# Performance work log

Measured on AMD Instinct MI355X. Metric: run time of the kernel, lower is better.

Reference implementation:

```python
import jax, jax.numpy as jnp
import numpy as np

BN_EPS = 1e-5


def setup_inputs() -> dict:
    key = jax.random.key(0)
    ks = jax.random.split(key, 8)
    B, C, H, W = 8, 256, 64, 64
    Cqk = C // 8  # query/key channels = out_channels // 8
    x = jax.random.normal(ks[0], (B, C, H, W), dtype=jnp.float32)
    # 1x1 convs == per-pixel matmuls; kaiming-normal-ish scale
    wq = jax.random.normal(ks[1], (Cqk, C), dtype=jnp.float32) * np.sqrt(2.0 / C)
    bq = jnp.zeros((Cqk,), dtype=jnp.float32)
    wk = jax.random.normal(ks[2], (Cqk, C), dtype=jnp.float32) * np.sqrt(2.0 / C)
    bk = jnp.zeros((Cqk,), dtype=jnp.float32)
    wv = jax.random.normal(ks[3], (C, C), dtype=jnp.float32) * np.sqrt(2.0 / C)
    bv = jnp.zeros((C,), dtype=jnp.float32)
    # gamma is initialized to 0 in the original; use a small nonzero value so
    # the attention path actually contributes (and has nontrivial gradients)
    gamma = jnp.full((1,), 0.5, dtype=jnp.float32)
    bn_weight = jnp.ones((C,), dtype=jnp.float32)
    bn_bias = jnp.zeros((C,), dtype=jnp.float32)
    return {"x": x, "wq": wq, "bq": bq, "wk": wk, "bk": bk,
            "wv": wv, "bv": bv, "gamma": gamma,
            "bn_weight": bn_weight, "bn_bias": bn_bias}


def reference(x, wq, bq, wk, bk, wv, bv, gamma, bn_weight, bn_bias):
    B, C, H, W = x.shape
    N = H * W
    xf = x.reshape(B, C, N)  # (B, C, N)
    # 1x1 conv projections as channel matmuls
    q = jnp.einsum('oc,bcn->bno', wq, xf) + bq            # (B, N, Cqk)
    k = jnp.einsum('oc,bcn->bon', wk, xf) + bk[:, None]   # (B, Cqk, N)
    v = jnp.einsum('oc,bcn->bon', wv, xf) + bv[:, None]   # (B, C, N)
    # attention[b, i, j] = softmax_j(q_i . k_j)  -- full N x N matrix
    scores = jnp.einsum('bno,bom->bnm', q, k)             # (B, N, N)
    attn = jax.nn.softmax(scores, axis=2)
    # out[b, c, i] = sum_j v[b, c, j] * attn[b, i, j]
    out = jnp.einsum('bcj,bij->bci', v, attn)             # (B, C, N)
    out = out.reshape(B, C, H, W)
    out = gamma[0] * out + x
    # BatchNorm2d in training mode: batch statistics over (B, H, W)
    mean = jnp.mean(out, axis=(0, 2, 3), keepdims=True)
    var = jnp.var(out, axis=(0, 2, 3), keepdims=True)
    out = (out - mean) * jax.lax.rsqrt(var + BN_EPS)
    out = out * bn_weight[None, :, None, None] + bn_bias[None, :, None, None]
    return jax.nn.relu(out)
```

## Files before the change

kernel.cpp:

```cpp
#include <hip/hip_runtime.h>
#include <stdint.h>

#define B_ 8
#define C_ 256
#define N_ 4096
#define CQK 32

typedef __attribute__((ext_vector_type(8))) _Float16 f16x8;
typedef __attribute__((ext_vector_type(4))) float f32x4;

__device__ __forceinline__ unsigned short f2bf_rne(float f) {
  unsigned u = __builtin_bit_cast(unsigned, f);
  u += 0x7FFFu + ((u >> 16) & 1u);
  return (unsigned short)(u >> 16);
}

__global__ __launch_bounds__(256) void xpose_kernel(
    const float* __restrict__ x, _Float16* __restrict__ xT)
{
  __shared__ float xs[64 * 129];
  const int t  = threadIdx.x;
  const int blk = blockIdx.x;
  const int nt = blk & 31;
  const int ct = (blk >> 5) & 3;
  const int b  = blk >> 7;
  const int c0 = ct * 64, n0 = nt * 128;

  #pragma unroll
  for (int p = 0; p < 8; ++p) {
    int cc = p * 8 + (t >> 5);
    int nn = (t & 31) * 4;
    float4 v = *(const float4*)(x + ((size_t)(b * C_ + c0 + cc)) * N_ + n0 + nn);
    xs[cc * 129 + nn]     = v.x;
    xs[cc * 129 + nn + 1] = v.y;
    xs[cc * 129 + nn + 2] = v.z;
    xs[cc * 129 + nn + 3] = v.w;
  }
  __syncthreads();
  #pragma unroll
  for (int p = 0; p < 4; ++p) {
    int id = p * 256 + t;
    int cchunk = id & 7, n = id >> 3;
    _Float16 h[8];
    #pragma unroll
    for (int j = 0; j < 8; ++j) h[j] = (_Float16)xs[(cchunk * 8 + j) * 129 + n];
    *(f16x8*)(xT + ((size_t)(b * N_) + n0 + n) * C_ + c0 + cchunk * 8) = *(f16x8*)h;
  }
}

__global__ __launch_bounds__(256) void wconv_kernel(
    const float* __restrict__ wq, const float* __restrict__ wk,
    const float* __restrict__ wv, _Float16* __restrict__ wf)
{
  int idx = blockIdx.x * 256 + threadIdx.x;
  int e = idx * 4;
  int o = e >> 8, c = e & 255;
  const float* src;
  if (o < 32)      src = wq + o * 256 + c;
  else if (o < 64) src = wk + (o - 32) * 256 + c;
  else             src = wv + (o - 64) * 256 + c;
  float4 v = *(const float4*)src;
  _Float16 h[4] = {(_Float16)v.x, (_Float16)v.y, (_Float16)v.z, (_Float16)v.w};
  *(uint2*)(wf + e) = *(uint2*)h;
}

__global__ __launch_bounds__(256, 4) void proj_gemm_kernel(
    const _Float16* __restrict__ xT, const _Float16* __restrict__ wf,
    const float* __restrict__ bq, const float* __restrict__ bk,
    const float* __restrict__ bv,
    _Float16* __restrict__ qf, _Float16* __restrict__ kf,
    _Float16* __restrict__ vout)
{
  const int t = threadIdx.x, lane = t & 63;
  const int w = t >> 6;
  const int l15 = lane & 15, q4 = lane >> 4;
  const int blk = blockIdx.x;
  const int otile = blk % 5;
  const int nt = blk / 5;
  const int b  = nt >> 5;
  const int n0 = (nt & 31) * 128;
  const int o0w = (w & 1) * 32;
  const int n0w = (w >> 1) * 64;

  f32x4 acc[2][4];
  const f32x4 zf = {0.f, 0.f, 0.f, 0.f};
  #pragma unroll
  for (int a = 0; a < 2; ++a)
    #pragma unroll
    for (int bb = 0; bb < 4; ++bb) acc[a][bb] = zf;

  const _Float16* wbase = wf + (size_t)(otile * 64 + o0w) * 256;
  const _Float16* xbase = xT + ((size_t)(b * N_) + n0 + n0w) * C_;

  #pragma unroll
  for (int kc = 0; kc < 8; ++kc) {
    f16x8 af[2], bfr[4];
    #pragma unroll
    for (int ob = 0; ob < 2; ++ob)
      af[ob] = *(const f16x8*)(wbase + (ob * 16 + l15) * 256 + kc * 32 + q4 * 8);
    #pragma unroll
    for (int nb = 0; nb < 4; ++nb)
      bfr[nb] = *(const f16x8*)(xbase + (nb * 16 + l15) * 256 + kc * 32 + q4 * 8);
    #pragma unroll
    for (int ob = 0; ob < 2; ++ob)
      #pragma unroll
      for (int nb = 0; nb < 4; ++nb)
        acc[ob][nb] = __builtin_amdgcn_mfma_f32_16x16x32_f16(af[ob], bfr[nb], acc[ob][nb], 0, 0, 0);
  }

  if (otile == 0) {
    _Float16* dst = (o0w == 0) ? qf : kf;
    const float* bias = (o0w == 0) ? bq : bk;
    const float qsc = (o0w == 0) ? 1.4426950408889634f : 1.0f;
    #pragma unroll
    for (int ob = 0; ob < 2; ++ob) {
      float4 b4 = *(const float4*)(bias + ob * 16 + q4 * 4);
      #pragma unroll
      for (int nb = 0; nb < 4; ++nb) {
        int pixel = n0 + n0w + nb * 16 + l15;
        _Float16 h[4];
        h[0] = (_Float16)((acc[ob][nb][0] + b4.x) * qsc);
        h[1] = (_Float16)((acc[ob][nb][1] + b4.y) * qsc);
        h[2] = (_Float16)((acc[ob][nb][2] + b4.z) * qsc);
        h[3] = (_Float16)((acc[ob][nb][3] + b4.w) * qsc);
        *(uint2*)(dst + ((size_t)(b * N_) + pixel) * CQK + ob * 16 + q4 * 4) = *(uint2*)h;
      }
    }
  } else {
    int cbase = (otile - 1) * 64 + o0w;
    #pragma unroll
    for (int ob = 0; ob < 2; ++ob) {
      float4 b4 = *(const float4*)(bv + cbase + ob * 16 + q4 * 4);
      #pragma unroll
      for (int nb = 0; nb < 4; ++nb) {
        int pixel = n0 + n0w + nb * 16 + l15;
        #pragma unroll
        for (int r = 0; r < 4; ++r) {
          int c = cbase + ob * 16 + q4 * 4 + r;
          float bval = (r == 0) ? b4.x : (r == 1) ? b4.y : (r == 2) ? b4.z : b4.w;
          vout[((size_t)(b * C_) + c) * N_ + pixel] = (_Float16)(acc[ob][nb][r] + bval);
        }
      }
    }
  }
}

#define ATTN_BODY(JT, KC, KN) do { \
  const int buf_ = (JT) & 1; \
   \
  f16x8 vv_[8]; \
  _Pragma("unroll") \
  for (int ks = 0; ks < 2; ++ks) { \
    vv_[ks * 4 + 0] = *(const f16x8*)(vp0 + ks * 32); \
    vv_[ks * 4 + 1] = *(const f16x8*)(vp1 + ks * 32); \
    vv_[ks * 4 + 2] = *(const f16x8*)(vp2 + ks * 32); \
    vv_[ks * 4 + 3] = *(const f16x8*)(vp3 + ks * 32); \
  } \
  vp0 += 64; vp1 += 64; vp2 += 64; vp3 += 64; \
   \
  { const _Float16* knp_ = kbase + (size_t)((((JT) + 1) & 63) * 64) * CQK; \
    _Pragma("unroll") \
    for (int jb = 0; jb < 4; ++jb) KN[jb] = *(const f16x8*)(knp_ + jb * 16 * CQK); } \
   \
  f32x4 sv_[4]; \
  _Pragma("unroll") \
  for (int jb = 0; jb < 4; ++jb) \
    sv_[jb] = __builtin_amdgcn_mfma_f32_16x16x32_f16(KC[jb], qfr, zf, 0, 0, 0); \
  float lm_ = sv_[0][0]; \
  _Pragma("unroll") \
  for (int jb = 0; jb < 4; ++jb) \
    lm_ = fmaxf(lm_, fmaxf(fmaxf(sv_[jb][0], sv_[jb][1]), fmaxf(sv_[jb][2], sv_[jb][3]))); \
  lm_ = fmaxf(lm_, __shfl_xor(lm_, 16)); \
  lm_ = fmaxf(lm_, __shfl_xor(lm_, 32)); \
  bool upd_ = lm_ > mold + 8.0f; \
  unsigned long long bal_ = __ballot(upd_);             \
  float alpha_ = upd_ ? exp2f(mold - lm_) : 1.0f; \
  if (upd_) mold = lm_; \
  float ts_ = 0.f; \
  float p_[4][4]; \
  _Pragma("unroll") \
  for (int jb = 0; jb < 4; ++jb) \
    _Pragma("unroll") \
    for (int r = 0; r < 4; ++r) { p_[jb][r] = exp2f(sv_[jb][r] - mold); ts_ += p_[jb][r]; } \
  ts_ += __shfl_xor(ts_, 16); \
  ts_ += __shfl_xor(ts_, 32); \
  lrun = lrun * alpha_ + ts_; \
  { char* pb_ = (char*)Plds + buf_ * 9216 + (w * 16 + l15) * 144 + q4 * 8; \
    _Pragma("unroll") \
    for (int jb = 0; jb < 4; ++jb) { \
      _Float16 h_[4] = {(_Float16)p_[jb][0], (_Float16)p_[jb][1], \
                        (_Float16)p_[jb][2], (_Float16)p_[jb][3]}; \
      *(uint2*)(pb_ + jb * 32) = *(uint2*)h_; } } \
  if (q4 == 0) alphal[buf_ * 64 + w * 16 + l15] = alpha_; \
  if (lane == 0) flagw[buf_ * 4 + w] = (bal_ != 0ull) ? 1 : 0; \
  __syncthreads(); \
  { int4 fl_ = *(const int4*)(flagw + buf_ * 4); \
    if (fl_.x | fl_.y | fl_.z | fl_.w) { \
      _Pragma("unroll") \
      for (int ib = 0; ib < 4; ++ib) { \
        float av_ = alphal[buf_ * 64 + ib * 16 + l15]; \
        _Pragma("unroll") \
        for (int cb = 0; cb < 4; ++cb) \
          _Pragma("unroll") \
          for (int r = 0; r < 4; ++r) acc[cb][ib][r] *= av_; } } } \
  __builtin_amdgcn_s_setprio(1); \
  _Pragma("unroll") \
  for (int ks = 0; ks < 2; ++ks) { \
    f16x8 pf_[4]; \
    _Pragma("unroll") \
    for (int ib = 0; ib < 4; ++ib) \
      pf_[ib] = *(const f16x8*)((char*)Plds + buf_ * 9216 + (ib * 16 + l15) * 144 + ks * 64 + q4 * 16); \
    _Pragma("unroll") \
    for (int cb = 0; cb < 4; ++cb) \
      _Pragma("unroll") \
      for (int ib = 0; ib < 4; ++ib) \
        acc[cb][ib] = __builtin_amdgcn_mfma_f32_16x16x32_f16(vv_[ks * 4 + cb], pf_[ib], acc[cb][ib], 0, 0, 0); \
  } \
  __builtin_amdgcn_s_setprio(0); \
} while (0)

__global__ __launch_bounds__(256, 2) void attn_kernel(
    const float* __restrict__ x, const float* __restrict__ gptr,
    const _Float16* __restrict__ qf, const _Float16* __restrict__ kf,
    const _Float16* __restrict__ vf, unsigned short* __restrict__ yout)
{
  __shared__ __align__(16) char smem[19232];
  _Float16* Plds  = (_Float16*)smem;
  float* alphal = (float*)(smem + 18432);
  int*   flagw  = (int*)(smem + 18944);
  float* lrowl  = (float*)(smem + 18976);

  const int t = threadIdx.x, lane = t & 63;
  const int w = t >> 6;
  const int l15 = lane & 15, q4 = lane >> 4;
  const int b  = blockIdx.x & 7;
  const int it = blockIdx.x >> 3;
  const int i0 = it * 64;
  const float gamma = gptr[0];

  const f16x8 qfr = *(const f16x8*)(qf + ((size_t)(b * N_) + i0 + w * 16 + l15) * CQK + q4 * 8);

  const _Float16* kbase = kf + ((size_t)(b * N_) + l15) * CQK + q4 * 8;
  const _Float16* vp0 = vf + ((size_t)(b * C_) + w * 64 + l15) * N_ + q4 * 8;
  const _Float16* vp1 = vp0 + (size_t)16 * N_;
  const _Float16* vp2 = vp0 + (size_t)32 * N_;
  const _Float16* vp3 = vp0 + (size_t)48 * N_;

  f32x4 acc[4][4];
  const f32x4 zf = {0.f, 0.f, 0.f, 0.f};
  #pragma unroll
  for (int a = 0; a < 4; ++a)
    #pragma unroll
    for (int bb = 0; bb < 4; ++bb) acc[a][bb] = zf;

  float mold = -1e30f, lrun = 0.f;

  f16x8 ka[4], kb[4];
  #pragma unroll
  for (int jb = 0; jb < 4; ++jb) ka[jb] = *(const f16x8*)(kbase + jb * 16 * CQK);

  #pragma unroll 1
  for (int jt = 0; jt < 64; jt += 2) {
    ATTN_BODY(jt, ka, kb);
    ATTN_BODY(jt + 1, kb, ka);
  }

  if (q4 == 0) lrowl[w * 16 + l15] = lrun;
  __syncthreads();
  #pragma unroll
  for (int ib = 0; ib < 4; ++ib) {
    float linv = 1.0f / lrowl[ib * 16 + l15];
    int i = i0 + ib * 16 + l15;
    #pragma unroll
    for (int cb = 0; cb < 4; ++cb) {
      #pragma unroll
      for (int r = 0; r < 4; ++r) {
        int c = w * 64 + cb * 16 + q4 * 4 + r;
        size_t off = ((size_t)(b * C_) + c) * N_ + i;
        float o = acc[cb][ib][r] * linv;
        yout[off] = f2bf_rne(fmaf(gamma, o, x[off]));
      }
    }
  }
}

__global__ __launch_bounds__(256) void bnstats_kernel(
    const unsigned short* __restrict__ y, float* __restrict__ meanw, float* __restrict__ rstdw)
{
  const int c = blockIdx.x;
  const int t = threadIdx.x;
  float s1 = 0.f, s2 = 0.f;
  for (int b = 0; b < B_; ++b) {
    const unsigned short* p = y + ((size_t)(b * C_ + c)) * N_;
    #pragma unroll
    for (int r = 0; r < 2; ++r) {
      uint4 u = *(const uint4*)(p + r * 2048 + t * 8);
      unsigned uu[4] = {u.x, u.y, u.z, u.w};
      #pragma unroll
      for (int k = 0; k < 4; ++k) {
        float a = __builtin_bit_cast(float, uu[k] << 16);
        float bb = __builtin_bit_cast(float, uu[k] & 0xFFFF0000u);
        s1 += a + bb;
        s2 += a * a + bb * bb;
      }
    }
  }
  __shared__ float r1[256], r2[256];
  r1[t] = s1; r2[t] = s2;
  __syncthreads();
  for (int s = 128; s > 0; s >>= 1) {
    if (t < s) { r1[t] += r1[t + s]; r2[t] += r2[t + s]; }
    __syncthreads();
  }
  if (t == 0) {
    float mean = r1[0] * (1.0f / 32768.0f);
    float var  = r2[0] * (1.0f / 32768.0f) - mean * mean;
    meanw[c] = mean;
    rstdw[c] = rsqrtf(var + 1e-5f);
  }
}

__global__ __launch_bounds__(256) void bnapply_kernel(
    const unsigned short* __restrict__ y, float* __restrict__ out,
    const float* __restrict__ meanw, const float* __restrict__ rstdw,
    const float* __restrict__ bnw, const float* __restrict__ bnb)
{
  size_t idx = (size_t)blockIdx.x * 256 + threadIdx.x;
  size_t el = idx * 8;
  int c = (int)((el >> 12) & 255);
  float sc = bnw[c] * rstdw[c];
  float sh = fmaf(-meanw[c], sc, bnb[c]);
  uint4 u = *(const uint4*)(y + el);
  unsigned uu[4] = {u.x, u.y, u.z, u.w};
  float4 o0, o1;
  float v[8];
  #pragma unroll
  for (int k = 0; k < 4; ++k) {
    v[2 * k]     = __builtin_bit_cast(float, uu[k] << 16);
    v[2 * k + 1] = __builtin_bit_cast(float, uu[k] & 0xFFFF0000u);
  }
  o0.x = fmaxf(fmaf(v[0], sc, sh), 0.f);
  o0.y = fmaxf(fmaf(v[1], sc, sh), 0.f);
  o0.z = fmaxf(fmaf(v[2], sc, sh), 0.f);
  o0.w = fmaxf(fmaf(v[3], sc, sh), 0.f);
  o1.x = fmaxf(fmaf(v[4], sc, sh), 0.f);
  o1.y = fmaxf(fmaf(v[5], sc, sh), 0.f);
  o1.z = fmaxf(fmaf(v[6], sc, sh), 0.f);
  o1.w = fmaxf(fmaf(v[7], sc, sh), 0.f);
  *(float4*)(out + el) = o0;
  *(float4*)(out + el + 4) = o1;
}

extern "C" void kernel_launch(void* const* d_in, const int* in_sizes, int n_in,
                              void* d_out, int out_size, void* d_ws, size_t ws_size,
                              hipStream_t stream)
{
  const float* x   = (const float*)d_in[0];
  const float* wq  = (const float*)d_in[1];
  const float* bq  = (const float*)d_in[2];
  const float* wk  = (const float*)d_in[3];
  const float* bk  = (const float*)d_in[4];
  const float* wv  = (const float*)d_in[5];
  const float* bv  = (const float*)d_in[6];
  const float* gm  = (const float*)d_in[7];
  const float* bnw = (const float*)d_in[8];
  const float* bnb = (const float*)d_in[9];
  float* out = (float*)d_out;

  _Float16* xT  = (_Float16*)d_out;
  _Float16* vfp = (_Float16*)((char*)d_out + (size_t)B_ * C_ * N_ * 2);

  char* ws = (char*)d_ws;
  _Float16* qf = (_Float16*)(ws);
  _Float16* kf = (_Float16*)(ws + ((size_t)2 << 20));
  unsigned short* yout = (unsigned short*)(ws + ((size_t)4 << 20));
  _Float16* wf = (_Float16*)(ws + ((size_t)21 << 20));
  float* meanw = (float*)(ws + ((size_t)22 << 20));
  float* rstdw = (float*)(ws + ((size_t)22 << 20) + 4096);

  hipLaunchKernelGGL(xpose_kernel, dim3(1024), dim3(256), 0, stream, x, xT);
  hipLaunchKernelGGL(wconv_kernel, dim3(80), dim3(256), 0, stream, wq, wk, wv, wf);
  hipLaunchKernelGGL(proj_gemm_kernel, dim3(1280), dim3(256), 0, stream,
                     xT, wf, bq, bk, bv, qf, kf, vfp);
  hipLaunchKernelGGL(attn_kernel, dim3(512), dim3(256), 0, stream,
                     x, gm, qf, kf, vfp, yout);
  hipLaunchKernelGGL(bnstats_kernel, dim3(256), dim3(256), 0, stream,
                     yout, meanw, rstdw);
  hipLaunchKernelGGL(bnapply_kernel, dim3(4096), dim3(256), 0, stream,
                     yout, out, meanw, rstdw, bnw, bnb);
}
```

Baseline: 302.4 us.

## Software-pipeline attention loop: overlap PV of tile k with softmax of tile k+1

Restructures the flash-attention main loop so each iteration consumes P of the previous tile (PV MFMAs) and then computes scores and softmax for the next tile, with a single lighter barrier per iteration. V fragments are double-buffered in registers, and K is prefetched two tiles ahead. The aim is to hide the softmax/LDS round-trip latency behind PV MFMAs and replace __syncthreads with an lgkmcnt wait plus s_barrier. The cost is more live registers (two V buffers of 8 f16x8 each), which could raise register pressure at 2 blocks per CU.

```diff
diff --git a/kernel.cpp b/kernel.cpp
--- a/kernel.cpp
+++ b/kernel.cpp
@@ -145,23 +145,40 @@
   }
 }
 
-#define ATTN_BODY(JT, KC, KN) do { \
-  const int buf_ = (JT) & 1; \
-   \
-  f16x8 vv_[8]; \
+#define BAR_PUB() do { \
+  asm volatile("s_waitcnt lgkmcnt(0)" ::: "memory"); \
+  __builtin_amdgcn_sched_barrier(0); \
+  __builtin_amdgcn_s_barrier(); \
+  asm volatile("" ::: "memory"); \
+} while (0)
+
+#define PV_CONS(RB, VC) do { \
+  int4 fl_ = *(const int4*)(flagw + (RB) * 4); \
+  if (fl_.x | fl_.y | fl_.z | fl_.w) { \
+    _Pragma("unroll") \
+    for (int ib = 0; ib < 4; ++ib) { \
+      float av_ = alphal[(RB) * 64 + ib * 16 + l15]; \
+      _Pragma("unroll") \
+      for (int cb = 0; cb < 4; ++cb) \
+        _Pragma("unroll") \
+        for (int r = 0; r < 4; ++r) acc[cb][ib][r] *= av_; } } \
+  __builtin_amdgcn_s_setprio(1); \
   _Pragma("unroll") \
   for (int ks = 0; ks < 2; ++ks) { \
-    vv_[ks * 4 + 0] = *(const f16x8*)(vp0 + ks * 32); \
-    vv_[ks * 4 + 1] = *(const f16x8*)(vp1 + ks * 32); \
-    vv_[ks * 4 + 2] = *(const f16x8*)(vp2 + ks * 32); \
-    vv_[ks * 4 + 3] = *(const f16x8*)(vp3 + ks * 32); \
+    f16x8 pf_[4]; \
+    _Pragma("unroll") \
+    for (int ib = 0; ib < 4; ++ib) \
+      pf_[ib] = *(const f16x8*)((char*)Plds + (RB) * 9216 + (ib * 16 + l15) * 144 + ks * 64 + q4 * 16); \
+    _Pragma("unroll") \
+    for (int cb = 0; cb < 4; ++cb) \
+      _Pragma("unroll") \
+      for (int ib = 0; ib < 4; ++ib) \
+        acc[cb][ib] = __builtin_amdgcn_mfma_f32_16x16x32_f16(VC[ks * 4 + cb], pf_[ib], acc[cb][ib], 0, 0, 0); \
   } \
-  vp0 += 64; vp1 += 64; vp2 += 64; vp3 += 64; \
-   \
-  { const _Float16* knp_ = kbase + (size_t)((((JT) + 1) & 63) * 64) * CQK; \
-    _Pragma("unroll") \
-    for (int jb = 0; jb < 4; ++jb) KN[jb] = *(const f16x8*)(knp_ + jb * 16 * CQK); } \
-   \
+  __builtin_amdgcn_s_setprio(0); \
+} while (0)
+
+#define SMAX_PUB(KC, WB) do { \
   f32x4 sv_[4]; \
   _Pragma("unroll") \
   for (int jb = 0; jb < 4; ++jb) \
@@ -173,7 +190,7 @@
   lm_ = fmaxf(lm_, __shfl_xor(lm_, 16)); \
   lm_ = fmaxf(lm_, __shfl_xor(lm_, 32)); \
   bool upd_ = lm_ > mold + 8.0f; \
-  unsigned long long bal_ = __ballot(upd_);             \
+  unsigned long long bal_ = __ballot(upd_); \
   float alpha_ = upd_ ? exp2f(mold - lm_) : 1.0f; \
   if (upd_) mold = lm_; \
   float ts_ = 0.f; \
@@ -185,38 +202,31 @@
   ts_ += __shfl_xor(ts_, 16); \
   ts_ += __shfl_xor(ts_, 32); \
   lrun = lrun * alpha_ + ts_; \
-  { char* pb_ = (char*)Plds + buf_ * 9216 + (w * 16 + l15) * 144 + q4 * 8; \
+  { char* pb_ = (char*)Plds + (WB) * 9216 + (w * 16 + l15) * 144 + q4 * 8; \
     _Pragma("unroll") \
     for (int jb = 0; jb < 4; ++jb) { \
       _Float16 h_[4] = {(_Float16)p_[jb][0], (_Float16)p_[jb][1], \
                         (_Float16)p_[jb][2], (_Float16)p_[jb][3]}; \
       *(uint2*)(pb_ + jb * 32) = *(uint2*)h_; } } \
-  if (q4 == 0) alphal[buf_ * 64 + w * 16 + l15] = alpha_; \
-  if (lane == 0) flagw[buf_ * 4 + w] = (bal_ != 0ull) ? 1 : 0; \
-  __syncthreads(); \
-  { int4 fl_ = *(const int4*)(flagw + buf_ * 4); \
-    if (fl_.x | fl_.y | fl_.z | fl_.w) { \
-      _Pragma("unroll") \
-      for (int ib = 0; ib < 4; ++ib) { \
-        float av_ = alphal[buf_ * 64 + ib * 16 + l15]; \
-        _Pragma("unroll") \
-        for (int cb = 0; cb < 4; ++cb) \
-          _Pragma("unroll") \
-          for (int r = 0; r < 4; ++r) acc[cb][ib][r] *= av_; } } } \
-  __builtin_amdgcn_s_setprio(1); \
+  if (q4 == 0) alphal[(WB) * 64 + w * 16 + l15] = alpha_; \
+  if (lane == 0) flagw[(WB) * 4 + w] = (bal_ != 0ull) ? 1 : 0; \
+} while (0)
+
+#define ATTN_BODY(K, VC, VN, KC, KN) do { \
   _Pragma("unroll") \
   for (int ks = 0; ks < 2; ++ks) { \
-    f16x8 pf_[4]; \
-    _Pragma("unroll") \
-    for (int ib = 0; ib < 4; ++ib) \
-      pf_[ib] = *(const f16x8*)((char*)Plds + buf_ * 9216 + (ib * 16 + l15) * 144 + ks * 64 + q4 * 16); \
-    _Pragma("unroll") \
-    for (int cb = 0; cb < 4; ++cb) \
-      _Pragma("unroll") \
-      for (int ib = 0; ib < 4; ++ib) \
-        acc[cb][ib] = __builtin_amdgcn_mfma_f32_16x16x32_f16(vv_[ks * 4 + cb], pf_[ib], acc[cb][ib], 0, 0, 0); \
+    VN[ks * 4 + 0] = *(const f16x8*)(vp0 + ks * 32); \
+    VN[ks * 4 + 1] = *(const f16x8*)(vp1 + ks * 32); \
+    VN[ks * 4 + 2] = *(const f16x8*)(vp2 + ks * 32); \
+    VN[ks * 4 + 3] = *(const f16x8*)(vp3 + ks * 32); \
   } \
-  __builtin_amdgcn_s_setprio(0); \
+  vp0 += 64; vp1 += 64; vp2 += 64; vp3 += 64; \
+  { const _Float16* knp_ = kbase + (size_t)((((K) + 2) & 63) * 64) * CQK; \
+    _Pragma("unroll") \
+    for (int jb = 0; jb < 4; ++jb) KN[jb] = *(const f16x8*)(knp_ + jb * 16 * CQK); } \
+  PV_CONS((K) & 1, VC); \
+  SMAX_PUB(KC, ((K) + 1) & 1); \
+  BAR_PUB(); \
 } while (0)
 
 __global__ __launch_bounds__(256, 2) void attn_kernel(
@@ -255,15 +265,30 @@
 
   float mold = -1e30f, lrun = 0.f;
 
-  f16x8 ka[4], kb[4];
+  f16x8 ka[4], kb[4], va[8], vb[8];
   #pragma unroll
   for (int jb = 0; jb < 4; ++jb) ka[jb] = *(const f16x8*)(kbase + jb * 16 * CQK);
+  #pragma unroll
+  for (int jb = 0; jb < 4; ++jb) kb[jb] = *(const f16x8*)(kbase + (size_t)(64 * CQK) + jb * 16 * CQK);
+  #pragma unroll
+  for (int ks = 0; ks < 2; ++ks) {
+    va[ks * 4 + 0] = *(const f16x8*)(vp0 + ks * 32);
+    va[ks * 4 + 1] = *(const f16x8*)(vp1 + ks * 32);
+    va[ks * 4 + 2] = *(const f16x8*)(vp2 + ks * 32);
+    va[ks * 4 + 3] = *(const f16x8*)(vp3 + ks * 32);
+  }
+  vp0 += 64; vp1 += 64; vp2 += 64; vp3 += 64;
+
+  SMAX_PUB(ka, 0);
+  BAR_PUB();
 
   #pragma unroll 1
-  for (int jt = 0; jt < 64; jt += 2) {
-    ATTN_BODY(jt, ka, kb);
-    ATTN_BODY(jt + 1, kb, ka);
-  }
+  for (int k = 0; k < 62; k += 2) {
+    ATTN_BODY(k,     va, vb, kb, ka);
+    ATTN_BODY(k + 1, vb, va, ka, kb);
+  }
+  ATTN_BODY(62, va, vb, kb, ka);
+  PV_CONS(1, vb);
 
   if (q4 == 0) lrowl[w * 16 + l15] = lrun;
   __syncthreads();
```

New measurement: 302.7 us. Within noise of the previous version (+0.1%).

## Store V in per-tile panels and process 128 keys per attention iteration

Applied to the files above, without the earlier changes.

The V projection output is rewritten into panels of 64 pixels by all channels, so each attention tile reads V from a contiguous region instead of rows strided by N. The attention loop now handles 128 keys per step, doubling the P buffer in LDS, with K loaded directly rather than software-prefetched. The syncthreads is replaced by an explicit lgkmcnt wait plus barrier. This halves the number of barriers and softmax reductions per row and improves V locality, at the cost of more registers and LDS, which may reduce occupancy, and of losing the K prefetch overlap.

```diff
diff --git a/kernel.cpp b/kernel.cpp
--- a/kernel.cpp
+++ b/kernel.cpp
@@ -5,6 +5,7 @@
 #define C_ 256
 #define N_ 4096
 #define CQK 32
+#define VPANEL (C_ * 64)
 
 typedef __attribute__((ext_vector_type(8))) _Float16 f16x8;
 typedef __attribute__((ext_vector_type(4))) float f32x4;
@@ -128,93 +129,95 @@
     }
   } else {
     int cbase = (otile - 1) * 64 + o0w;
+    const int panel = (n0 + n0w) >> 6;
+    _Float16* vpan = vout + ((size_t)(b * 64 + panel)) * VPANEL;
     #pragma unroll
     for (int ob = 0; ob < 2; ++ob) {
       float4 b4 = *(const float4*)(bv + cbase + ob * 16 + q4 * 4);
       #pragma unroll
       for (int nb = 0; nb < 4; ++nb) {
-        int pixel = n0 + n0w + nb * 16 + l15;
+        int jj = nb * 16 + l15;
         #pragma unroll
         for (int r = 0; r < 4; ++r) {
           int c = cbase + ob * 16 + q4 * 4 + r;
           float bval = (r == 0) ? b4.x : (r == 1) ? b4.y : (r == 2) ? b4.z : b4.w;
-          vout[((size_t)(b * C_) + c) * N_ + pixel] = (_Float16)(acc[ob][nb][r] + bval);
+          vpan[(size_t)c * 64 + jj] = (_Float16)(acc[ob][nb][r] + bval);
         }
       }
     }
   }
 }
 
-#define ATTN_BODY(JT, KC, KN) do { \
-  const int buf_ = (JT) & 1; \
-   \
-  f16x8 vv_[8]; \
+#define ATTN_BODY(K, BUF) do { \
+   \
+  f16x8 kx_[8]; \
+  { const _Float16* kp_ = kbase + (size_t)(K) * 128 * CQK; \
+    _Pragma("unroll") \
+    for (int jb = 0; jb < 8; ++jb) kx_[jb] = *(const f16x8*)(kp_ + jb * 16 * CQK); } \
+   \
+  f16x8 vx_[16]; \
+  { const _Float16* vp_ = vbase + (size_t)(K) * 2 * VPANEL; \
+    _Pragma("unroll") \
+    for (int ks = 0; ks < 4; ++ks) \
+      _Pragma("unroll") \
+      for (int cb = 0; cb < 4; ++cb) \
+        vx_[ks * 4 + cb] = *(const f16x8*)(vp_ + (ks >> 1) * VPANEL + cb * 1024 + (ks & 1) * 32); } \
+   \
+  f32x4 sv_[8]; \
   _Pragma("unroll") \
-  for (int ks = 0; ks < 2; ++ks) { \
-    vv_[ks * 4 + 0] = *(const f16x8*)(vp0 + ks * 32); \
-    vv_[ks * 4 + 1] = *(const f16x8*)(vp1 + ks * 32); \
-    vv_[ks * 4 + 2] = *(const f16x8*)(vp2 + ks * 32); \
-    vv_[ks * 4 + 3] = *(const f16x8*)(vp3 + ks * 32); \
-  } \
-  vp0 += 64; vp1 += 64; vp2 += 64; vp3 += 64; \
-   \
-  { const _Float16* knp_ = kbase + (size_t)((((JT) + 1) & 63) * 64) * CQK; \
-    _Pragma("unroll") \
-    for (int jb = 0; jb < 4; ++jb) KN[jb] = *(const f16x8*)(knp_ + jb * 16 * CQK); } \
-   \
-  f32x4 sv_[4]; \
-  _Pragma("unroll") \
-  for (int jb = 0; jb < 4; ++jb) \
-    sv_[jb] = __builtin_amdgcn_mfma_f32_16x16x32_f16(KC[jb], qfr, zf, 0, 0, 0); \
+  for (int jb = 0; jb < 8; ++jb) \
+    sv_[jb] = __builtin_amdgcn_mfma_f32_16x16x32_f16(kx_[jb], qfr, zf, 0, 0, 0); \
   float lm_ = sv_[0][0]; \
   _Pragma("unroll") \
-  for (int jb = 0; jb < 4; ++jb) \
+  for (int jb = 0; jb < 8; ++jb) \
     lm_ = fmaxf(lm_, fmaxf(fmaxf(sv_[jb][0], sv_[jb][1]), fmaxf(sv_[jb][2], sv_[jb][3]))); \
   lm_ = fmaxf(lm_, __shfl_xor(lm_, 16)); \
   lm_ = fmaxf(lm_, __shfl_xor(lm_, 32)); \
   bool upd_ = lm_ > mold + 8.0f; \
-  unsigned long long bal_ = __ballot(upd_);             \
+  unsigned long long bal_ = __ballot(upd_);      \
   float alpha_ = upd_ ? exp2f(mold - lm_) : 1.0f; \
   if (upd_) mold = lm_; \
   float ts_ = 0.f; \
-  float p_[4][4]; \
-  _Pragma("unroll") \
-  for (int jb = 0; jb < 4; ++jb) \
-    _Pragma("unroll") \
-    for (int r = 0; r < 4; ++r) { p_[jb][r] = exp2f(sv_[jb][r] - mold); ts_ += p_[jb][r]; } \
+  { char* pb_ = (char*)Plds + (BUF) * 17408 + (w * 16 + l15) * 272 + q4 * 8; \
+    _Pragma("unroll") \
+    for (int jb = 0; jb < 8; ++jb) { \
+      float p0_ = exp2f(sv_[jb][0] - mold), p1_ = exp2f(sv_[jb][1] - mold); \
+      float p2_ = exp2f(sv_[jb][2] - mold), p3_ = exp2f(sv_[jb][3] - mold); \
+      ts_ += (p0_ + p1_) + (p2_ + p3_); \
+      _Float16 h_[4] = {(_Float16)p0_, (_Float16)p1_, (_Float16)p2_, (_Float16)p3_}; \
+      *(uint2*)(pb_ + jb * 32) = *(uint2*)h_; } } \
+  if (q4 == 0) alphal[(BUF) * 64 + w * 16 + l15] = alpha_; \
+  if (lane == 0) flagw[(BUF) * 4 + w] = (bal_ != 0ull) ? 1 : 0; \
   ts_ += __shfl_xor(ts_, 16); \
   ts_ += __shfl_xor(ts_, 32); \
   lrun = lrun * alpha_ + ts_; \
-  { char* pb_ = (char*)Plds + buf_ * 9216 + (w * 16 + l15) * 144 + q4 * 8; \
-    _Pragma("unroll") \
-    for (int jb = 0; jb < 4; ++jb) { \
-      _Float16 h_[4] = {(_Float16)p_[jb][0], (_Float16)p_[jb][1], \
-                        (_Float16)p_[jb][2], (_Float16)p_[jb][3]}; \
-      *(uint2*)(pb_ + jb * 32) = *(uint2*)h_; } } \
-  if (q4 == 0) alphal[buf_ * 64 + w * 16 + l15] = alpha_; \
-  if (lane == 0) flagw[buf_ * 4 + w] = (bal_ != 0ull) ? 1 : 0; \
-  __syncthreads(); \
-  { int4 fl_ = *(const int4*)(flagw + buf_ * 4); \
+  asm volatile("s_waitcnt lgkmcnt(0)" ::: "memory"); \
+  __builtin_amdgcn_sched_barrier(0); \
+  __builtin_amdgcn_s_barrier(); \
+  asm volatile("" ::: "memory"); \
+   \
+  { int4 fl_ = *(const int4*)(flagw + (BUF) * 4); \
     if (fl_.x | fl_.y | fl_.z | fl_.w) { \
       _Pragma("unroll") \
       for (int ib = 0; ib < 4; ++ib) { \
-        float av_ = alphal[buf_ * 64 + ib * 16 + l15]; \
+        float av_ = alphal[(BUF) * 64 + ib * 16 + l15]; \
         _Pragma("unroll") \
         for (int cb = 0; cb < 4; ++cb) \
           _Pragma("unroll") \
           for (int r = 0; r < 4; ++r) acc[cb][ib][r] *= av_; } } } \
+   \
   __builtin_amdgcn_s_setprio(1); \
   _Pragma("unroll") \
-  for (int ks = 0; ks < 2; ++ks) { \
+  for (int ks = 0; ks < 4; ++ks) { \
     f16x8 pf_[4]; \
     _Pragma("unroll") \
     for (int ib = 0; ib < 4; ++ib) \
-      pf_[ib] = *(const f16x8*)((char*)Plds + buf_ * 9216 + (ib * 16 + l15) * 144 + ks * 64 + q4 * 16); \
+      pf_[ib] = *(const f16x8*)((char*)Plds + (BUF) * 17408 + (ib * 16 + l15) * 272 + ks * 64 + q4 * 16); \
     _Pragma("unroll") \
     for (int cb = 0; cb < 4; ++cb) \
       _Pragma("unroll") \
       for (int ib = 0; ib < 4; ++ib) \
-        acc[cb][ib] = __builtin_amdgcn_mfma_f32_16x16x32_f16(vv_[ks * 4 + cb], pf_[ib], acc[cb][ib], 0, 0, 0); \
+        acc[cb][ib] = __builtin_amdgcn_mfma_f32_16x16x32_f16(vx_[ks * 4 + cb], pf_[ib], acc[cb][ib], 0, 0, 0); \
   } \
   __builtin_amdgcn_s_setprio(0); \
 } while (0)
@@ -224,11 +227,11 @@
     const _Float16* __restrict__ qf, const _Float16* __restrict__ kf,
     const _Float16* __restrict__ vf, unsigned short* __restrict__ yout)
 {
-  __shared__ __align__(16) char smem[19232];
+  __shared__ __align__(16) char smem[35648];
   _Float16* Plds  = (_Float16*)smem;
-  float* alphal = (float*)(smem + 18432);
-  int*   flagw  = (int*)(smem + 18944);
-  float* lrowl  = (float*)(smem + 18976);
+  float* alphal = (float*)(smem + 34816);
+  int*   flagw  = (int*)(smem + 35328);
+  float* lrowl  = (float*)(smem + 35360);
 
   const int t = threadIdx.x, lane = t & 63;
   const int w = t >> 6;
@@ -241,10 +244,8 @@
   const f16x8 qfr = *(const f16x8*)(qf + ((size_t)(b * N_) + i0 + w * 16 + l15) * CQK + q4 * 8);
 
   const _Float16* kbase = kf + ((size_t)(b * N_) + l15) * CQK + q4 * 8;
-  const _Float16* vp0 = vf + ((size_t)(b * C_) + w * 64 + l15) * N_ + q4 * 8;
-  const _Float16* vp1 = vp0 + (size_t)16 * N_;
-  const _Float16* vp2 = vp0 + (size_t)32 * N_;
-  const _Float16* vp3 = vp0 + (size_t)48 * N_;
+  const _Float16* vbase = vf + (size_t)b * (64 * VPANEL)
+                             + ((size_t)(w * 64 + l15)) * 64 + q4 * 8;
 
   f32x4 acc[4][4];
   const f32x4 zf = {0.f, 0.f, 0.f, 0.f};
@@ -255,14 +256,10 @@
 
   float mold = -1e30f, lrun = 0.f;
 
-  f16x8 ka[4], kb[4];
-  #pragma unroll
-  for (int jb = 0; jb < 4; ++jb) ka[jb] = *(const f16x8*)(kbase + jb * 16 * CQK);
-
   #pragma unroll 1
-  for (int jt = 0; jt < 64; jt += 2) {
-    ATTN_BODY(jt, ka, kb);
-    ATTN_BODY(jt + 1, kb, ka);
+  for (int k = 0; k < 32; k += 2) {
+    ATTN_BODY(k, 0);
+    ATTN_BODY(k + 1, 1);
   }
 
   if (q4 == 0) lrowl[w * 16 + l15] = lrun;
```

Result: no change. 297.8 us (-1.5%).
